# Performance work log

Hardware: AMD Instinct MI355X
Metric: run time of the kernel (lower is better)

## Reference

```python
import jax, jax.numpy as jnp
import numpy as np
import math

L = 24  # legendre_polys; output features = L*L = 576


def _sh_norm(l, m):
    # exact Python-int factorial ratio, then sqrt (same as original)
    return math.sqrt((2.0 * l + 1.0) * math.factorial(l - m) / (4 * math.pi * math.factorial(l + m)))


def setup_inputs() -> dict:
    key = jax.random.key(0)
    u = jax.random.uniform(key, (400000, 2), dtype=jnp.float32)
    ra = u[:, 0] * 360.0          # degrees [0, 360)
    dec = u[:, 1] * 180.0 - 90.0  # degrees [-90, 90)
    return {"ra_dec": jnp.stack([ra, dec], axis=1)}


def reference(ra_dec):
    ra, dec = ra_dec[:, 0], ra_dec[:, 1]
    phi = jnp.deg2rad(ra)
    theta = jnp.deg2rad(dec + 90.0)
    x = jnp.cos(theta)                      # [N]
    somx2 = jnp.sqrt((1.0 - x) * (1.0 + x))  # sin(theta) magnitude

    # Associated Legendre P_l^m(x) for all 0 <= m <= l < L via the SAME
    # recursion as the original (computed once per (l,m) instead of from
    # scratch each call -- identical math, O(L^2) total).
    P = {}
    pmm = jnp.ones_like(x)
    fact = 1.0
    for m in range(L):
        if m > 0:
            pmm = pmm * (-fact) * somx2  # P_m^m
            fact += 2.0
        P[(m, m)] = pmm
        if m + 1 < L:
            cur = x * (2.0 * m + 1.0) * pmm  # P_{m+1}^m
            P[(m + 1, m)] = cur
            prev = pmm
            for ll in range(m + 2, L):
                nxt = ((2.0 * ll - 1.0) * x * cur - (ll + m - 1.0) * prev) / (ll - m)
                P[(ll, m)] = nxt
                prev, cur = cur, nxt

    sqrt2 = math.sqrt(2.0)
    Y = []
    for l in range(L):
        for m in range(-l, l + 1):
            am = abs(m)
            K = _sh_norm(l, am)
            if m == 0:
                y = K * P[(l, 0)]
            elif m > 0:
                y = sqrt2 * K * jnp.cos(m * phi) * P[(l, m)]
            else:
                y = sqrt2 * K * jnp.sin(am * phi) * P[(l, am)]
            Y.append(y)
    return jnp.stack(Y, axis=-1)  # [N, L*L]
```

## Files before the change

### kernel.cpp

```cpp
#include <hip/hip_runtime.h>
#include <type_traits>

#define LMAX 24

constexpr double csqrt_(double x) {
  double y = x > 1.0 ? x : 1.0;
  for (int i = 0; i < 300; ++i) y = 0.5 * (y + x / y);
  return y;
}
constexpr double cfact_(int n) {
  double r = 1.0;
  for (int i = 2; i <= n; ++i) r *= (double)i;
  return r;
}
constexpr double PI_ = 3.14159265358979323846;

struct KTab {
  float k[LMAX][LMAX];
  constexpr KTab() : k{} {
    for (int l = 0; l < LMAX; ++l)
      for (int m = 0; m <= l; ++m)
        k[l][m] = (float)csqrt_((2.0 * l + 1.0) * cfact_(l - m) /
                                (4.0 * PI_ * cfact_(l + m)));
  }
};
constexpr KTab KT{};
constexpr float SQRT2_ = 1.41421356237309504880f;

template <int N, int I = 0, typename F>
__device__ __forceinline__ void static_for(F&& f) {
  if constexpr (I < N) {
    f(std::integral_constant<int, I>{});
    static_for<N, I + 1>(f);
  }
}

#define CJ 32
#define STR 33

__global__ __launch_bounds__(256) void sh_kernel(const float* __restrict__ rd,
                                                 float* __restrict__ out, int n) {
  __shared__ float lds[4 * 64 * STR];

  const int tid = threadIdx.x;
  const int wave = tid >> 6;
  const int lane = tid & 63;
  const long long base_pt = (long long)blockIdx.x * 256 + wave * 64;
  const long long my_pt = base_pt + lane;
  const int src = my_pt < n ? (int)my_pt : 0;

  const float2 p = reinterpret_cast<const float2*>(rd)[src];
  const float D2R = 0.017453292519943295f;
  float phi = p.x * D2R;
  float theta = (p.y + 90.0f) * D2R;
  float x = cosf(theta);
  float somx2 = sqrtf((1.0f - x) * (1.0f + x));

  float cm[LMAX], sm[LMAX];
  cm[0] = 1.0f; sm[0] = 0.0f;
  float c1 = cosf(phi), s1 = sinf(phi);
  cm[1] = c1; sm[1] = s1;
  float twoc = 2.0f * c1;
#pragma unroll
  for (int m = 2; m < LMAX; ++m) {
    cm[m] = twoc * cm[m - 1] - cm[m - 2];
    sm[m] = twoc * sm[m - 1] - sm[m - 2];
  }

  float cur[LMAX], prev[LMAX];
  float pmm = 1.0f;

  float* const wptr = lds + wave * (64 * STR) + lane * STR;
  const float* const rbase = lds + wave * (64 * STR);

  auto flush = [&](int jc) {
    __builtin_amdgcn_wave_barrier();
#pragma unroll
    for (int t = 0; t < 8; ++t) {
      int pp = t * 8 + (lane >> 3);
      int off = pp * STR + (lane & 7) * 4;
      float4 v = make_float4(rbase[off], rbase[off + 1],
                             rbase[off + 2], rbase[off + 3]);
      long long pt = base_pt + pp;
      if (pt < n) {
        *reinterpret_cast<float4*>(out + (size_t)pt * (LMAX * LMAX) +
                                   jc * CJ + (lane & 7) * 4) = v;
      }
    }
    __builtin_amdgcn_wave_barrier();
  };

  static_for<LMAX>([&](auto LC) {
    constexpr int l = decltype(LC)::value;

    static_for<l>([&](auto MC) {
      constexpr int m = decltype(MC)::value;
      constexpr float a = (float)(2 * l - 1);
      constexpr float b = (float)(l + m - 1);
      constexpr float inv = 1.0f / (float)(l - m);
      float nxt = (a * x * cur[m] - b * prev[m]) * inv;
      prev[m] = cur[m];
      cur[m] = nxt;
    });

    if constexpr (l > 0) {
      pmm = pmm * (-(float)(2 * l - 1)) * somx2;
    }
    cur[l] = pmm;
    prev[l] = 0.0f;

    static_for<2 * l + 1>([&](auto KC) {
      constexpr int m = decltype(KC)::value - l;
      constexpr int am = m < 0 ? -m : m;
      constexpr int j = l * l + l + m;
      constexpr float C = (m == 0) ? KT.k[l][0] : SQRT2_ * KT.k[l][am];
      float y;
      if constexpr (m == 0) {
        y = C * cur[0];
      } else if constexpr (m > 0) {
        y = C * (cm[am] * cur[am]);
      } else {
        y = C * (sm[am] * cur[am]);
      }
      wptr[j & (CJ - 1)] = y;
      if constexpr ((j & (CJ - 1)) == CJ - 1) {
        flush(j >> 5);
      }
    });
  });
}

extern "C" void kernel_launch(void* const* d_in, const int* in_sizes, int n_in,
                              void* d_out, int out_size, void* d_ws, size_t ws_size,
                              hipStream_t stream) {
  (void)n_in; (void)out_size; (void)d_ws; (void)ws_size;
  const float* rd = (const float*)d_in[0];
  float* out = (float*)d_out;
  int n = in_sizes[0] / 2;
  int grid = (n + 255) / 256;
  sh_kernel<<<grid, 256, 0, stream>>>(rd, out, n);
}
```

Measured before the change: 187.9 us.

## Vectorize LDS staging with float4, add nontemporal stores and fast sincos

Changes the LDS row stride from 33 to 36 so each point's row is 16-byte aligned. Per-point values are packed into float4 LDS writes and read back as float4. Global output writes use nontemporal stores, and full waves skip the per-point bounds check. __sincosf replaces separate cosf/sinf, which trades some accuracy for cheaper trig. The aims are fewer LDS instructions and less cache pollution from the large streamed output, at some risk of LDS bank conflicts with the new stride.

```diff
diff --git a/kernel.cpp b/kernel.cpp
--- a/kernel.cpp
+++ b/kernel.cpp
@@ -2,6 +2,8 @@
 #include <type_traits>
 
 #define LMAX 24
+
+typedef float f32x4 __attribute__((ext_vector_type(4)));
 
 constexpr double csqrt_(double x) {
   double y = x > 1.0 ? x : 1.0;
@@ -36,7 +38,7 @@
 }
 
 #define CJ 32
-#define STR 33
+#define STR 36
 
 __global__ __launch_bounds__(256) void sh_kernel(const float* __restrict__ rd,
                                                  float* __restrict__ out, int n) {
@@ -48,6 +50,7 @@
   const long long base_pt = (long long)blockIdx.x * 256 + wave * 64;
   const long long my_pt = base_pt + lane;
   const int src = my_pt < n ? (int)my_pt : 0;
+  const bool full = (base_pt + 64) <= (long long)n;
 
   const float2 p = reinterpret_cast<const float2*>(rd)[src];
   const float D2R = 0.017453292519943295f;
@@ -58,7 +61,8 @@
 
   float cm[LMAX], sm[LMAX];
   cm[0] = 1.0f; sm[0] = 0.0f;
-  float c1 = cosf(phi), s1 = sinf(phi);
+  float c1, s1;
+  __sincosf(phi, &s1, &c1);
   cm[1] = c1; sm[1] = s1;
   float twoc = 2.0f * c1;
 #pragma unroll
@@ -69,22 +73,35 @@
 
   float cur[LMAX], prev[LMAX];
   float pmm = 1.0f;
+  float buf[4];
 
   float* const wptr = lds + wave * (64 * STR) + lane * STR;
   const float* const rbase = lds + wave * (64 * STR);
 
   auto flush = [&](int jc) {
     __builtin_amdgcn_wave_barrier();
+    if (full) {
 #pragma unroll
-    for (int t = 0; t < 8; ++t) {
-      int pp = t * 8 + (lane >> 3);
-      int off = pp * STR + (lane & 7) * 4;
-      float4 v = make_float4(rbase[off], rbase[off + 1],
-                             rbase[off + 2], rbase[off + 3]);
-      long long pt = base_pt + pp;
-      if (pt < n) {
-        *reinterpret_cast<float4*>(out + (size_t)pt * (LMAX * LMAX) +
-                                   jc * CJ + (lane & 7) * 4) = v;
+      for (int t = 0; t < 8; ++t) {
+        int pp = t * 8 + (lane >> 3);
+        int off = pp * STR + (lane & 7) * 4;
+        f32x4 v = *reinterpret_cast<const f32x4*>(rbase + off);
+        __builtin_nontemporal_store(
+            v, reinterpret_cast<f32x4*>(out + (base_pt + pp) * (size_t)(LMAX * LMAX) +
+                                        jc * CJ + (lane & 7) * 4));
+      }
+    } else {
+#pragma unroll
+      for (int t = 0; t < 8; ++t) {
+        int pp = t * 8 + (lane >> 3);
+        int off = pp * STR + (lane & 7) * 4;
+        f32x4 v = *reinterpret_cast<const f32x4*>(rbase + off);
+        long long pt = base_pt + pp;
+        if (pt < n) {
+          __builtin_nontemporal_store(
+              v, reinterpret_cast<f32x4*>(out + pt * (size_t)(LMAX * LMAX) +
+                                          jc * CJ + (lane & 7) * 4));
+        }
       }
     }
     __builtin_amdgcn_wave_barrier();
@@ -122,7 +139,11 @@
       } else {
         y = C * (sm[am] * cur[am]);
       }
-      wptr[j & (CJ - 1)] = y;
+      buf[j & 3] = y;
+      if constexpr ((j & 3) == 3) {
+        *reinterpret_cast<f32x4*>(wptr + ((j & (CJ - 1)) & ~3)) =
+            f32x4{buf[0], buf[1], buf[2], buf[3]};
+      }
       if constexpr ((j & (CJ - 1)) == CJ - 1) {
         flush(j >> 5);
       }
```

Result: slower. 194.9 us (+3.7%).
